# Performance work log

Measured on AMD Instinct MI355X. Metric: run time of the kernel, lower is better.

## Reference

```python
import jax, jax.numpy as jnp
import numpy as np
from jax import lax

T, B, H, HID = 1024, 64, 512, 512
EPS = 1e-5


def _lstm_scan(xs, Wx, Wh, b):
    # xs: [T, B, H] time-major; returns hidden states [T, B, HID]
    bsz = xs.shape[1]
    c0 = jnp.zeros((bsz, Wh.shape[0]), xs.dtype)
    h0 = jnp.zeros_like(c0)

    def step(carry, x):
        c, h = carry
        z = x @ Wx + h @ Wh + b  # [B, 4*HID]
        i, f, g, o = jnp.split(z, 4, axis=-1)  # flax gate order i, f, g, o
        c = jax.nn.sigmoid(f) * c + jax.nn.sigmoid(i) * jnp.tanh(g)
        h = jax.nn.sigmoid(o) * jnp.tanh(c)
        return (c, h), h

    _, hs = lax.scan(step, (c0, h0), xs)
    return hs


def _flip_sequences(x_bth, lengths):
    # x_bth: [B, T, H]; keep padding at the end while reversing valid prefix.
    max_len = x_bth.shape[1]
    return jax.vmap(lambda x, l: jnp.flip(jnp.roll(x, max_len - l, axis=0), axis=0))(
        x_bth, lengths)


def setup_inputs() -> dict:
    key = jax.random.key(0)
    ks = jax.random.split(key, 12)
    inputs = jax.random.normal(ks[0], (T, B, H), jnp.float32)
    lengths = jax.random.randint(ks[1], (B,), T // 2, T + 1).astype(jnp.int32)
    t_idx = jnp.arange(T)[:, None]
    mask = (t_idx < lengths[None, :]).astype(jnp.float32).reshape(T * B, 1)
    # BatchNorm params
    scale = 1.0 + 0.1 * jax.random.normal(ks[2], (H,), jnp.float32)
    bias = 0.1 * jax.random.normal(ks[3], (H,), jnp.float32)
    sx = 1.0 / np.sqrt(H)
    sh = 1.0 / np.sqrt(HID)
    Wx_f = sx * jax.random.normal(ks[4], (H, 4 * HID), jnp.float32)
    Wh_f = sh * jax.random.normal(ks[5], (HID, 4 * HID), jnp.float32)
    b_f = jnp.zeros((4 * HID,), jnp.float32)
    Wx_b = sx * jax.random.normal(ks[6], (H, 4 * HID), jnp.float32)
    Wh_b = sh * jax.random.normal(ks[7], (HID, 4 * HID), jnp.float32)
    b_b = jnp.zeros((4 * HID,), jnp.float32)
    return {
        "inputs": inputs, "lengths": lengths, "mask": mask,
        "scale": scale, "bias": bias,
        "Wx_f": Wx_f, "Wh_f": Wh_f, "b_f": b_f,
        "Wx_b": Wx_b, "Wh_b": Wh_b, "b_b": b_b,
        "training": 1,
    }


def reference(inputs, lengths, mask, scale, bias,
              Wx_f, Wh_f, b_f, Wx_b, Wh_b, b_b, training):
    t, n, h = inputs.shape
    x = inputs.reshape(t * n, h)
    if training:
        # masked batch statistics (matches flax BatchNorm override)
        non_zeros = jnp.sum(mask, axis=0)  # [1]
        mean = jnp.sum(x, axis=0) / non_zeros  # [H]
        mean2 = jnp.sum(lax.square(x), axis=0) / non_zeros
        var = jnp.maximum(0.0, mean2 - lax.square(mean))
    else:
        mean = jnp.zeros((h,), jnp.float32)
        var = jnp.ones((h,), jnp.float32)
    y = (x - mean) * lax.rsqrt(var + EPS) * scale + bias
    y = (y * mask).reshape(t, n, h)  # [T, B, H]

    # forward direction
    fwd = _lstm_scan(y, Wx_f, Wh_f, b_f)  # [T, B, HID]
    # backward direction on length-aware flipped inputs
    rev_in = _flip_sequences(y.transpose(1, 0, 2), lengths).transpose(1, 0, 2)
    bwd = _lstm_scan(rev_in, Wx_b, Wh_b, b_b)
    bwd = _flip_sequences(bwd.transpose(1, 0, 2), lengths).transpose(1, 0, 2)
    return fwd + bwd  # [T, B, HID]
```

## Files before the change

kernel.cpp:

```cpp
#include <hip/hip_runtime.h>
#include <math.h>

#define T_DIM 1024
#define B_DIM 64
#define H_DIM 512
#define HID   512
#define EPS_F 1e-5f

#define WS_SUM    0
#define WS_SUMSQ  512
#define WS_A      1024
#define WS_C0     1536
#define WS_HBUF   4096
#define WS_CBUF   (4096 + 131072)
#define WS_XZ     (4096 + 131072 + 65536)
#define WS_END    (WS_XZ + 524288)

__device__ __forceinline__ float sigf(float v) {
    return 1.0f / (1.0f + __expf(-v));
}

__global__ void stats_kernel(const float* __restrict__ x, float* __restrict__ ws) {
    int col = blockIdx.x * 256 + threadIdx.x;
    int row0 = blockIdx.y * 512;
    float s = 0.f, s2 = 0.f;
    for (int r = 0; r < 512; ++r) {
        float v = x[(size_t)(row0 + r) * H_DIM + col];
        s += v;
        s2 += v * v;
    }
    atomicAdd(&ws[WS_SUM + col], s);
    atomicAdd(&ws[WS_SUMSQ + col], s2);
}

__global__ void finalize_kernel(const int* __restrict__ lengths,
                                const float* __restrict__ scale,
                                const float* __restrict__ bias,
                                const int* __restrict__ training,
                                float* __restrict__ ws) {
    __shared__ float cnt_sh;
    int tid = threadIdx.x;
    if (tid == 0) {
        int c = 0;
        for (int b = 0; b < B_DIM; ++b) c += lengths[b];
        cnt_sh = (float)c;
    }
    __syncthreads();
    float a, c0;
    if (*training) {
        float inv = 1.0f / cnt_sh;
        float mean = ws[WS_SUM + tid] * inv;
        float mean2 = ws[WS_SUMSQ + tid] * inv;
        float var = fmaxf(0.0f, mean2 - mean * mean);
        a = scale[tid] * rsqrtf(var + EPS_F);
        c0 = bias[tid] - mean * a;
    } else {
        a = scale[tid] * rsqrtf(1.0f + EPS_F);
        c0 = bias[tid];
    }
    ws[WS_A + tid] = a;
    ws[WS_C0 + tid] = c0;
}

__launch_bounds__(256)
__global__ void step_kernel(int t,
                            const float* __restrict__ x,
                            const int* __restrict__ lengths,
                            const float* __restrict__ mask,
                            const float* __restrict__ Wx_f, const float* __restrict__ Wh_f,
                            const float* __restrict__ b_f,
                            const float* __restrict__ Wx_b, const float* __restrict__ Wh_b,
                            const float* __restrict__ b_b,
                            float* __restrict__ ws, float* __restrict__ out) {
    __shared__ __align__(16) float As[64 * 68];
    __shared__ __align__(16) float Ws_[64 * 68];

    const int role = blockIdx.x >> 6;
    const int r6   = blockIdx.x & 63;
    const int dir  = r6 >> 5;
    const int jt   = r6 & 31;
    const int tid  = threadIdx.x;
    const int tidb = tid & 15;
    const int tidn = tid >> 4;
    const int b0   = tidb << 2;
    const int n0   = tidn << 2;

    const int target = t + 1;
    if (role == 0 && t < 0) return;
    if (role == 1 && target >= T_DIM) return;

    const int g   = tidn >> 2;
    const int jj0 = (tidn & 3) << 2;
    const int col_base = g * 512 + jt * 16 + jj0;

    const float* W  = (role == 1) ? (dir ? Wx_b : Wx_f) : (dir ? Wh_b : Wh_f);
    const float* bv = dir ? b_b : b_f;

    float acc[4][4];
    if (role == 0) {
        const int xzb = ((t & 1) * 2 + dir) * (B_DIM * 2048);
#pragma unroll
        for (int i = 0; i < 4; ++i) {
            float4 v = *reinterpret_cast<const float4*>(&ws[WS_XZ + xzb + (b0 + i) * 2048 + col_base]);
            acc[i][0] = v.x; acc[i][1] = v.y; acc[i][2] = v.z; acc[i][3] = v.w;
        }
    } else {
        float4 bvv = *reinterpret_cast<const float4*>(&bv[col_base]);
#pragma unroll
        for (int i = 0; i < 4; ++i) {
            acc[i][0] = bvv.x; acc[i][1] = bvv.y; acc[i][2] = bvv.z; acc[i][3] = bvv.w;
        }
    }

    const int hbase_in = ((t & 1) * 2 + dir) * (B_DIM * 512);

    for (int ck = 0; ck < 8; ++ck) {
        const int k0c = ck * 64;
#pragma unroll
        for (int i = 0; i < 4; ++i) {
            int f4  = tid + i * 256;
            int kk4 = f4 & 15;
            int b   = f4 >> 4;
            int k   = k0c + (kk4 << 2);
            float4 v;
            if (role == 0) {
                v = *reinterpret_cast<const float4*>(&ws[WS_HBUF + hbase_in + b * 512 + k]);
            } else {
                int trow;
                if (dir == 0) {
                    trow = target;
                } else {
                    trow = lengths[b] - 1 - target;
                    if (trow < 0) trow += T_DIM;
                }
                float4 xv = *reinterpret_cast<const float4*>(&x[((size_t)trow * B_DIM + b) * H_DIM + k]);
                float  m  = mask[(size_t)trow * B_DIM + b];
                float4 av = *reinterpret_cast<const float4*>(&ws[WS_A + k]);
                float4 cv = *reinterpret_cast<const float4*>(&ws[WS_C0 + k]);
                v.x = (xv.x * av.x + cv.x) * m;
                v.y = (xv.y * av.y + cv.y) * m;
                v.z = (xv.z * av.z + cv.z) * m;
                v.w = (xv.w * av.w + cv.w) * m;
            }
            int kr = kk4 << 2;
            As[(kr + 0) * 68 + b] = v.x;
            As[(kr + 1) * 68 + b] = v.y;
            As[(kr + 2) * 68 + b] = v.z;
            As[(kr + 3) * 68 + b] = v.w;
        }
#pragma unroll
        for (int i = 0; i < 4; ++i) {
            int f4  = tid + i * 256;
            int n4  = f4 & 15;
            int kk  = f4 >> 4;
            int nl  = n4 << 2;
            int gg  = nl >> 4;
            int jj  = nl & 15;
            int colw = gg * 512 + jt * 16 + jj;
            float4 wv = *reinterpret_cast<const float4*>(&W[(size_t)(k0c + kk) * 2048 + colw]);
            *reinterpret_cast<float4*>(&Ws_[kk * 68 + nl]) = wv;
        }
        __syncthreads();
#pragma unroll 4
        for (int kk = 0; kk < 64; ++kk) {
            const float4 a4 = *reinterpret_cast<const float4*>(&As[kk * 68 + b0]);
            const float4 w4 = *reinterpret_cast<const float4*>(&Ws_[kk * 68 + n0]);
            acc[0][0] += a4.x * w4.x; acc[0][1] += a4.x * w4.y; acc[0][2] += a4.x * w4.z; acc[0][3] += a4.x * w4.w;
            acc[1][0] += a4.y * w4.x; acc[1][1] += a4.y * w4.y; acc[1][2] += a4.y * w4.z; acc[1][3] += a4.y * w4.w;
            acc[2][0] += a4.z * w4.x; acc[2][1] += a4.z * w4.y; acc[2][2] += a4.z * w4.z; acc[2][3] += a4.z * w4.w;
            acc[3][0] += a4.w * w4.x; acc[3][1] += a4.w * w4.y; acc[3][2] += a4.w * w4.z; acc[3][3] += a4.w * w4.w;
        }
        __syncthreads();
    }

    if (role == 1) {
        const int xzb = ((target & 1) * 2 + dir) * (B_DIM * 2048);
#pragma unroll
        for (int i = 0; i < 4; ++i) {
            float4 v = make_float4(acc[i][0], acc[i][1], acc[i][2], acc[i][3]);
            *reinterpret_cast<float4*>(&ws[WS_XZ + xzb + (b0 + i) * 2048 + col_base]) = v;
        }
        return;
    }

    float* zs = As;
#pragma unroll
    for (int i = 0; i < 4; ++i) {
        float4 v = make_float4(acc[i][0], acc[i][1], acc[i][2], acc[i][3]);
        *reinterpret_cast<float4*>(&zs[(b0 + i) * 68 + n0]) = v;
    }
    __syncthreads();

    const int b   = tid >> 2;
    const int jjg = (tid & 3) << 2;
    const int hc  = jt * 16 + jjg;

    float4 zi = *reinterpret_cast<const float4*>(&zs[b * 68 +  0 + jjg]);
    float4 zf = *reinterpret_cast<const float4*>(&zs[b * 68 + 16 + jjg]);
    float4 zg = *reinterpret_cast<const float4*>(&zs[b * 68 + 32 + jjg]);
    float4 zo = *reinterpret_cast<const float4*>(&zs[b * 68 + 48 + jjg]);

    float* cptr = &ws[WS_CBUF + (dir * B_DIM + b) * 512 + hc];
    float4 c4 = *reinterpret_cast<const float4*>(cptr);

    float cn[4], hv[4];
    {
        float c = sigf(zf.x) * c4.x + sigf(zi.x) * tanhf(zg.x);
        cn[0] = c; hv[0] = sigf(zo.x) * tanhf(c);
    }
    {
        float c = sigf(zf.y) * c4.y + sigf(zi.y) * tanhf(zg.y);
        cn[1] = c; hv[1] = sigf(zo.y) * tanhf(c);
    }
    {
        float c = sigf(zf.z) * c4.z + sigf(zi.z) * tanhf(zg.z);
        cn[2] = c; hv[2] = sigf(zo.z) * tanhf(c);
    }
    {
        float c = sigf(zf.w) * c4.w + sigf(zi.w) * tanhf(zg.w);
        cn[3] = c; hv[3] = sigf(zo.w) * tanhf(c);
    }

    *reinterpret_cast<float4*>(cptr) = make_float4(cn[0], cn[1], cn[2], cn[3]);

    const int hbase_out = (((t + 1) & 1) * 2 + dir) * (B_DIM * 512);
    *reinterpret_cast<float4*>(&ws[WS_HBUF + hbase_out + b * 512 + hc]) =
        make_float4(hv[0], hv[1], hv[2], hv[3]);

    int orow;
    if (dir == 0) {
        orow = t;
    } else {
        orow = lengths[b] - 1 - t;
        if (orow < 0) orow += T_DIM;
    }
    float* op = &out[((size_t)orow * B_DIM + b) * HID + hc];
    atomicAdd(&op[0], hv[0]);
    atomicAdd(&op[1], hv[1]);
    atomicAdd(&op[2], hv[2]);
    atomicAdd(&op[3], hv[3]);
}

extern "C" void kernel_launch(void* const* d_in, const int* in_sizes, int n_in,
                              void* d_out, int out_size, void* d_ws, size_t ws_size,
                              hipStream_t stream) {
    const float* x        = (const float*)d_in[0];
    const int*   lengths  = (const int*)d_in[1];
    const float* mask     = (const float*)d_in[2];
    const float* scale    = (const float*)d_in[3];
    const float* bias     = (const float*)d_in[4];
    const float* Wx_f     = (const float*)d_in[5];
    const float* Wh_f     = (const float*)d_in[6];
    const float* b_f      = (const float*)d_in[7];
    const float* Wx_b     = (const float*)d_in[8];
    const float* Wh_b     = (const float*)d_in[9];
    const float* b_b      = (const float*)d_in[10];
    const int*   training = (const int*)d_in[11];
    float* ws  = (float*)d_ws;
    float* out = (float*)d_out;

    hipMemsetAsync(ws, 0, (size_t)WS_END * sizeof(float), stream);
    hipMemsetAsync(out, 0, (size_t)out_size * sizeof(float), stream);

    stats_kernel<<<dim3(2, 128), 256, 0, stream>>>(x, ws);
    finalize_kernel<<<1, 512, 0, stream>>>(lengths, scale, bias, training, ws);

    for (int t = -1; t < T_DIM; ++t) {
        step_kernel<<<128, 256, 0, stream>>>(t, x, lengths, mask,
                                             Wx_f, Wh_f, b_f, Wx_b, Wh_b, b_b,
                                             ws, out);
    }
}
```

Baseline: 40.12 ms.

## Replace per-step launches with a persistent cooperative kernel using grid sync

Merges the stats, finalize and 1025 per-timestep launches into one cooperative kernel of 256 blocks that loops over time and separates steps with grid.sync. Half the blocks run the recurrent h·Wh update with split-K across 8 waves and a shared-memory reduction. The other blocks normalize and transpose the input and compute the x·Wx projection two stages ahead, replacing the mask read with a length comparison. The aim is to remove kernel launch overhead and overlap the input projection with the recurrence. The cost is a grid-wide barrier every step, and the weights are now read straight from global memory with no shared-memory tiling.

```diff
diff --git a/kernel.cpp b/kernel.cpp
--- a/kernel.cpp
+++ b/kernel.cpp
@@ -1,244 +1,221 @@
 #include <hip/hip_runtime.h>
+#include <hip/hip_cooperative_groups.h>
 #include <math.h>
+
+namespace cg = cooperative_groups;
 
 #define T_DIM 1024
 #define B_DIM 64
 #define H_DIM 512
-#define HID   512
 #define EPS_F 1e-5f
 
 #define WS_SUM    0
 #define WS_SUMSQ  512
-#define WS_A      1024
-#define WS_C0     1536
-#define WS_HBUF   4096
-#define WS_CBUF   (4096 + 131072)
-#define WS_XZ     (4096 + 131072 + 65536)
-#define WS_END    (WS_XZ + 524288)
+#define WS_HT     1024
+#define WS_CT     (WS_HT + 131072)
+#define WS_XZ     (WS_CT + 65536)
+#define WS_YT     (WS_XZ + 524288)
+#define WS_END    (WS_YT + 131072)
+#define WS_ZERO_END WS_XZ
 
 __device__ __forceinline__ float sigf(float v) {
     return 1.0f / (1.0f + __expf(-v));
 }
 
-__global__ void stats_kernel(const float* __restrict__ x, float* __restrict__ ws) {
-    int col = blockIdx.x * 256 + threadIdx.x;
-    int row0 = blockIdx.y * 512;
-    float s = 0.f, s2 = 0.f;
-    for (int r = 0; r < 512; ++r) {
-        float v = x[(size_t)(row0 + r) * H_DIM + col];
-        s += v;
-        s2 += v * v;
+__global__ __launch_bounds__(512)
+void brnn_persistent(const float* __restrict__ x, const int* __restrict__ lengths,
+                     const float* __restrict__ scale, const float* __restrict__ bias,
+                     const float* __restrict__ Wx_f, const float* __restrict__ Wh_f,
+                     const float* __restrict__ b_f,
+                     const float* __restrict__ Wx_b, const float* __restrict__ Wh_b,
+                     const float* __restrict__ b_b,
+                     const int* __restrict__ training,
+                     float* __restrict__ ws, float* __restrict__ out) {
+    cg::grid_group grid = cg::this_grid();
+
+    __shared__ union {
+        float red[8 * 2080];
+        float tile[512 * 9];
+    } U;
+    __shared__ float a_sh[512], c0_sh[512];
+    __shared__ int lsh[64];
+
+    const int tid = threadIdx.x;
+    const int bid = blockIdx.x;
+
+    {
+        float s = 0.f, s2 = 0.f;
+        const float* xp = x + (size_t)bid * 256 * 512 + tid;
+#pragma unroll 8
+        for (int r = 0; r < 256; ++r) {
+            float v = xp[(size_t)r * 512];
+            s += v; s2 += v * v;
+        }
+        atomicAdd(&ws[WS_SUM + tid], s);
+        atomicAdd(&ws[WS_SUMSQ + tid], s2);
     }
-    atomicAdd(&ws[WS_SUM + col], s);
-    atomicAdd(&ws[WS_SUMSQ + col], s2);
-}
-
-__global__ void finalize_kernel(const int* __restrict__ lengths,
-                                const float* __restrict__ scale,
-                                const float* __restrict__ bias,
-                                const int* __restrict__ training,
-                                float* __restrict__ ws) {
-    __shared__ float cnt_sh;
-    int tid = threadIdx.x;
-    if (tid == 0) {
-        int c = 0;
-        for (int b = 0; b < B_DIM; ++b) c += lengths[b];
-        cnt_sh = (float)c;
+    grid.sync();
+
+    if (tid < 64) lsh[tid] = lengths[tid];
+    __syncthreads();
+    {
+        float cnt = 0.f;
+        for (int b = 0; b < 64; ++b) cnt += (float)lsh[b];
+        float a, c0;
+        if (*training) {
+            float inv = 1.0f / cnt;
+            float mean = ws[WS_SUM + tid] * inv;
+            float mean2 = ws[WS_SUMSQ + tid] * inv;
+            float var = fmaxf(0.f, mean2 - mean * mean);
+            a = scale[tid] * rsqrtf(var + EPS_F);
+            c0 = bias[tid] - mean * a;
+        } else {
+            a = scale[tid] * rsqrtf(1.0f + EPS_F);
+            c0 = bias[tid];
+        }
+        a_sh[tid] = a;
+        c0_sh[tid] = c0;
     }
     __syncthreads();
-    float a, c0;
-    if (*training) {
-        float inv = 1.0f / cnt_sh;
-        float mean = ws[WS_SUM + tid] * inv;
-        float mean2 = ws[WS_SUMSQ + tid] * inv;
-        float var = fmaxf(0.0f, mean2 - mean * mean);
-        a = scale[tid] * rsqrtf(var + EPS_F);
-        c0 = bias[tid] - mean * a;
-    } else {
-        a = scale[tid] * rsqrtf(1.0f + EPS_F);
-        c0 = bias[tid];
+
+    const int w = __builtin_amdgcn_readfirstlane(tid >> 6);
+    const int lane = tid & 63;
+    const int kbase = w * 64;
+
+    for (int i = -2; i <= 1023; ++i) {
+        if (bid < 128) {
+            if (i >= 0) {
+                const int dir = bid >> 6;
+                const int hb = bid & 63;
+                const int hbase = hb << 3;
+                const int p = i & 1;
+                const float* __restrict__ Wh = dir ? Wh_b : Wh_f;
+                const float* arow = ws + WS_HT + ((size_t)(p * 2 + dir) * 512 + kbase) * 64 + lane;
+                const float* wp = Wh + (size_t)kbase * 2048 + hbase;
+                float acc[32];
+#pragma unroll
+                for (int c = 0; c < 32; ++c) acc[c] = 0.f;
+#pragma unroll 4
+                for (int kk = 0; kk < 64; ++kk) {
+                    float av = arow[kk * 64];
+                    const float* wr = wp + (size_t)kk * 2048;
+#pragma unroll
+                    for (int g = 0; g < 4; ++g)
+#pragma unroll
+                        for (int j = 0; j < 8; ++j)
+                            acc[g * 8 + j] = fmaf(wr[g * 512 + j], av, acc[g * 8 + j]);
+                }
+                __syncthreads();
+#pragma unroll
+                for (int c = 0; c < 32; ++c) U.red[w * 2080 + c * 65 + lane] = acc[c];
+                __syncthreads();
+                const int b = tid & 63;
+                const int h8 = tid >> 6;
+                const int hid = hbase + h8;
+                const float* xzp = ws + WS_XZ + (size_t)(p * 2 + dir) * 2048 * 64;
+                float z[4];
+#pragma unroll
+                for (int g = 0; g < 4; ++g) {
+                    float s = 0.f;
+#pragma unroll
+                    for (int w8 = 0; w8 < 8; ++w8)
+                        s += U.red[w8 * 2080 + (g * 8 + h8) * 65 + b];
+                    z[g] = s + xzp[(size_t)(g * 512 + hid) * 64 + b];
+                }
+                float* cp = ws + WS_CT + (size_t)(dir * 512 + hid) * 64 + b;
+                float cold = *cp;
+                float ig = sigf(z[0]), fg = sigf(z[1]);
+                float gg = tanhf(z[2]), og = sigf(z[3]);
+                float cn = fg * cold + ig * gg;
+                float hv = og * tanhf(cn);
+                *cp = cn;
+                ws[WS_HT + (size_t)(((p ^ 1) * 2 + dir) * 512 + hid) * 64 + b] = hv;
+                int orow;
+                if (dir == 0) orow = i;
+                else { orow = lsh[b] - 1 - i; if (orow < 0) orow += T_DIM; }
+                atomicAdd(&out[((size_t)orow * 64 + b) * 512 + hid], hv);
+            }
+        } else {
+            if (bid < 144 && i <= 1021) {
+                const int idx = bid - 128;
+                const int dir2 = idx & 1, bo = idx >> 1;
+                const int ttgt = i + 2;
+#pragma unroll
+                for (int it = 0; it < 2; ++it) {
+                    int id2 = tid + it * 512;
+                    int row = id2 >> 7;
+                    int k4 = id2 & 127;
+                    int b = bo * 8 + row;
+                    int l = lsh[b];
+                    int trow = dir2 ? (l - 1 - ttgt) : ttgt;
+                    if (trow < 0) trow += T_DIM;
+                    float m = (trow < l) ? 1.f : 0.f;
+                    const float4 xv = *reinterpret_cast<const float4*>(
+                        &x[((size_t)trow * 64 + b) * 512 + k4 * 4]);
+                    float4 a4 = *reinterpret_cast<const float4*>(&a_sh[k4 * 4]);
+                    float4 c4 = *reinterpret_cast<const float4*>(&c0_sh[k4 * 4]);
+                    U.tile[(k4 * 4 + 0) * 9 + row] = (xv.x * a4.x + c4.x) * m;
+                    U.tile[(k4 * 4 + 1) * 9 + row] = (xv.y * a4.y + c4.y) * m;
+                    U.tile[(k4 * 4 + 2) * 9 + row] = (xv.z * a4.z + c4.z) * m;
+                    U.tile[(k4 * 4 + 3) * 9 + row] = (xv.w * a4.w + c4.w) * m;
+                }
+                __syncthreads();
+                const int q2 = ttgt & 1;
+                float* yt = ws + WS_YT + (size_t)(q2 * 2 + dir2) * 512 * 64;
+#pragma unroll
+                for (int it = 0; it < 8; ++it) {
+                    int gid = tid + it * 512;
+                    int b = gid & 7;
+                    int k = gid >> 3;
+                    yt[(size_t)k * 64 + bo * 8 + b] = U.tile[k * 9 + b];
+                }
+                __syncthreads();
+            }
+            if (i >= -1 && i <= 1022) {
+                const int idx = bid - 128;
+                const int dir = idx >> 6;
+                const int cb = idx & 63;
+                const int colbase = cb << 5;
+                const int tt = i + 1;
+                const int q = tt & 1;
+                const float* __restrict__ Wx = dir ? Wx_b : Wx_f;
+                const float* __restrict__ bv = dir ? b_b : b_f;
+                const float* arow = ws + WS_YT + ((size_t)(q * 2 + dir) * 512 + kbase) * 64 + lane;
+                const float* wp = Wx + (size_t)kbase * 2048 + colbase;
+                float acc[32];
+#pragma unroll
+                for (int c = 0; c < 32; ++c) acc[c] = 0.f;
+#pragma unroll 4
+                for (int kk = 0; kk < 64; ++kk) {
+                    float av = arow[kk * 64];
+                    const float* wr = wp + (size_t)kk * 2048;
+#pragma unroll
+                    for (int c = 0; c < 32; ++c)
+                        acc[c] = fmaf(wr[c], av, acc[c]);
+                }
+                __syncthreads();
+#pragma unroll
+                for (int c = 0; c < 32; ++c) U.red[w * 2080 + c * 65 + lane] = acc[c];
+                __syncthreads();
+                const int co2 = tid >> 4;
+                const int b4 = (tid & 15) << 2;
+                float bb = bv[colbase + co2];
+                float r[4];
+#pragma unroll
+                for (int j = 0; j < 4; ++j) {
+                    float s = 0.f;
+#pragma unroll
+                    for (int w8 = 0; w8 < 8; ++w8)
+                        s += U.red[w8 * 2080 + co2 * 65 + b4 + j];
+                    r[j] = s + bb;
+                }
+                *reinterpret_cast<float4*>(
+                    &ws[WS_XZ + ((size_t)(q * 2 + dir) * 2048 + colbase + co2) * 64 + b4]) =
+                    make_float4(r[0], r[1], r[2], r[3]);
+            }
+        }
+        grid.sync();
     }
-    ws[WS_A + tid] = a;
-    ws[WS_C0 + tid] = c0;
-}
-
-__launch_bounds__(256)
-__global__ void step_kernel(int t,
-                            const float* __restrict__ x,
-                            const int* __restrict__ lengths,
-                            const float* __restrict__ mask,
-                            const float* __restrict__ Wx_f, const float* __restrict__ Wh_f,
-                            const float* __restrict__ b_f,
-                            const float* __restrict__ Wx_b, const float* __restrict__ Wh_b,
-                            const float* __restrict__ b_b,
-                            float* __restrict__ ws, float* __restrict__ out) {
-    __shared__ __align__(16) float As[64 * 68];
-    __shared__ __align__(16) float Ws_[64 * 68];
-
-    const int role = blockIdx.x >> 6;
-    const int r6   = blockIdx.x & 63;
-    const int dir  = r6 >> 5;
-    const int jt   = r6 & 31;
-    const int tid  = threadIdx.x;
-    const int tidb = tid & 15;
-    const int tidn = tid >> 4;
-    const int b0   = tidb << 2;
-    const int n0   = tidn << 2;
-
-    const int target = t + 1;
-    if (role == 0 && t < 0) return;
-    if (role == 1 && target >= T_DIM) return;
-
-    const int g   = tidn >> 2;
-    const int jj0 = (tidn & 3) << 2;
-    const int col_base = g * 512 + jt * 16 + jj0;
-
-    const float* W  = (role == 1) ? (dir ? Wx_b : Wx_f) : (dir ? Wh_b : Wh_f);
-    const float* bv = dir ? b_b : b_f;
-
-    float acc[4][4];
-    if (role == 0) {
-        const int xzb = ((t & 1) * 2 + dir) * (B_DIM * 2048);
-#pragma unroll
-        for (int i = 0; i < 4; ++i) {
-            float4 v = *reinterpret_cast<const float4*>(&ws[WS_XZ + xzb + (b0 + i) * 2048 + col_base]);
-            acc[i][0] = v.x; acc[i][1] = v.y; acc[i][2] = v.z; acc[i][3] = v.w;
-        }
-    } else {
-        float4 bvv = *reinterpret_cast<const float4*>(&bv[col_base]);
-#pragma unroll
-        for (int i = 0; i < 4; ++i) {
-            acc[i][0] = bvv.x; acc[i][1] = bvv.y; acc[i][2] = bvv.z; acc[i][3] = bvv.w;
-        }
-    }
-
-    const int hbase_in = ((t & 1) * 2 + dir) * (B_DIM * 512);
-
-    for (int ck = 0; ck < 8; ++ck) {
-        const int k0c = ck * 64;
-#pragma unroll
-        for (int i = 0; i < 4; ++i) {
-            int f4  = tid + i * 256;
-            int kk4 = f4 & 15;
-            int b   = f4 >> 4;
-            int k   = k0c + (kk4 << 2);
-            float4 v;
-            if (role == 0) {
-                v = *reinterpret_cast<const float4*>(&ws[WS_HBUF + hbase_in + b * 512 + k]);
-            } else {
-                int trow;
-                if (dir == 0) {
-                    trow = target;
-                } else {
-                    trow = lengths[b] - 1 - target;
-                    if (trow < 0) trow += T_DIM;
-                }
-                float4 xv = *reinterpret_cast<const float4*>(&x[((size_t)trow * B_DIM + b) * H_DIM + k]);
-                float  m  = mask[(size_t)trow * B_DIM + b];
-                float4 av = *reinterpret_cast<const float4*>(&ws[WS_A + k]);
-                float4 cv = *reinterpret_cast<const float4*>(&ws[WS_C0 + k]);
-                v.x = (xv.x * av.x + cv.x) * m;
-                v.y = (xv.y * av.y + cv.y) * m;
-                v.z = (xv.z * av.z + cv.z) * m;
-                v.w = (xv.w * av.w + cv.w) * m;
-            }
-            int kr = kk4 << 2;
-            As[(kr + 0) * 68 + b] = v.x;
-            As[(kr + 1) * 68 + b] = v.y;
-            As[(kr + 2) * 68 + b] = v.z;
-            As[(kr + 3) * 68 + b] = v.w;
-        }
-#pragma unroll
-        for (int i = 0; i < 4; ++i) {
-            int f4  = tid + i * 256;
-            int n4  = f4 & 15;
-            int kk  = f4 >> 4;
-            int nl  = n4 << 2;
-            int gg  = nl >> 4;
-            int jj  = nl & 15;
-            int colw = gg * 512 + jt * 16 + jj;
-            float4 wv = *reinterpret_cast<const float4*>(&W[(size_t)(k0c + kk) * 2048 + colw]);
-            *reinterpret_cast<float4*>(&Ws_[kk * 68 + nl]) = wv;
-        }
-        __syncthreads();
-#pragma unroll 4
-        for (int kk = 0; kk < 64; ++kk) {
-            const float4 a4 = *reinterpret_cast<const float4*>(&As[kk * 68 + b0]);
-            const float4 w4 = *reinterpret_cast<const float4*>(&Ws_[kk * 68 + n0]);
-            acc[0][0] += a4.x * w4.x; acc[0][1] += a4.x * w4.y; acc[0][2] += a4.x * w4.z; acc[0][3] += a4.x * w4.w;
-            acc[1][0] += a4.y * w4.x; acc[1][1] += a4.y * w4.y; acc[1][2] += a4.y * w4.z; acc[1][3] += a4.y * w4.w;
-            acc[2][0] += a4.z * w4.x; acc[2][1] += a4.z * w4.y; acc[2][2] += a4.z * w4.z; acc[2][3] += a4.z * w4.w;
-            acc[3][0] += a4.w * w4.x; acc[3][1] += a4.w * w4.y; acc[3][2] += a4.w * w4.z; acc[3][3] += a4.w * w4.w;
-        }
-        __syncthreads();
-    }
-
-    if (role == 1) {
-        const int xzb = ((target & 1) * 2 + dir) * (B_DIM * 2048);
-#pragma unroll
-        for (int i = 0; i < 4; ++i) {
-            float4 v = make_float4(acc[i][0], acc[i][1], acc[i][2], acc[i][3]);
-            *reinterpret_cast<float4*>(&ws[WS_XZ + xzb + (b0 + i) * 2048 + col_base]) = v;
-        }
-        return;
-    }
-
-    float* zs = As;
-#pragma unroll
-    for (int i = 0; i < 4; ++i) {
-        float4 v = make_float4(acc[i][0], acc[i][1], acc[i][2], acc[i][3]);
-        *reinterpret_cast<float4*>(&zs[(b0 + i) * 68 + n0]) = v;
-    }
-    __syncthreads();
-
-    const int b   = tid >> 2;
-    const int jjg = (tid & 3) << 2;
-    const int hc  = jt * 16 + jjg;
-
-    float4 zi = *reinterpret_cast<const float4*>(&zs[b * 68 +  0 + jjg]);
-    float4 zf = *reinterpret_cast<const float4*>(&zs[b * 68 + 16 + jjg]);
-    float4 zg = *reinterpret_cast<const float4*>(&zs[b * 68 + 32 + jjg]);
-    float4 zo = *reinterpret_cast<const float4*>(&zs[b * 68 + 48 + jjg]);
-
-    float* cptr = &ws[WS_CBUF + (dir * B_DIM + b) * 512 + hc];
-    float4 c4 = *reinterpret_cast<const float4*>(cptr);
-
-    float cn[4], hv[4];
-    {
-        float c = sigf(zf.x) * c4.x + sigf(zi.x) * tanhf(zg.x);
-        cn[0] = c; hv[0] = sigf(zo.x) * tanhf(c);
-    }
-    {
-        float c = sigf(zf.y) * c4.y + sigf(zi.y) * tanhf(zg.y);
-        cn[1] = c; hv[1] = sigf(zo.y) * tanhf(c);
-    }
-    {
-        float c = sigf(zf.z) * c4.z + sigf(zi.z) * tanhf(zg.z);
-        cn[2] = c; hv[2] = sigf(zo.z) * tanhf(c);
-    }
-    {
-        float c = sigf(zf.w) * c4.w + sigf(zi.w) * tanhf(zg.w);
-        cn[3] = c; hv[3] = sigf(zo.w) * tanhf(c);
-    }
-
-    *reinterpret_cast<float4*>(cptr) = make_float4(cn[0], cn[1], cn[2], cn[3]);
-
-    const int hbase_out = (((t + 1) & 1) * 2 + dir) * (B_DIM * 512);
-    *reinterpret_cast<float4*>(&ws[WS_HBUF + hbase_out + b * 512 + hc]) =
-        make_float4(hv[0], hv[1], hv[2], hv[3]);
-
-    int orow;
-    if (dir == 0) {
-        orow = t;
-    } else {
-        orow = lengths[b] - 1 - t;
-        if (orow < 0) orow += T_DIM;
-    }
-    float* op = &out[((size_t)orow * B_DIM + b) * HID + hc];
-    atomicAdd(&op[0], hv[0]);
-    atomicAdd(&op[1], hv[1]);
-    atomicAdd(&op[2], hv[2]);
-    atomicAdd(&op[3], hv[3]);
 }
 
 extern "C" void kernel_launch(void* const* d_in, const int* in_sizes, int n_in,
@@ -246,7 +223,6 @@
                               hipStream_t stream) {
     const float* x        = (const float*)d_in[0];
     const int*   lengths  = (const int*)d_in[1];
-    const float* mask     = (const float*)d_in[2];
     const float* scale    = (const float*)d_in[3];
     const float* bias     = (const float*)d_in[4];
     const float* Wx_f     = (const float*)d_in[5];
@@ -259,15 +235,15 @@
     float* ws  = (float*)d_ws;
     float* out = (float*)d_out;
 
-    hipMemsetAsync(ws, 0, (size_t)WS_END * sizeof(float), stream);
+    hipMemsetAsync(ws, 0, (size_t)WS_ZERO_END * sizeof(float), stream);
     hipMemsetAsync(out, 0, (size_t)out_size * sizeof(float), stream);
 
-    stats_kernel<<<dim3(2, 128), 256, 0, stream>>>(x, ws);
-    finalize_kernel<<<1, 512, 0, stream>>>(lengths, scale, bias, training, ws);
-
-    for (int t = -1; t < T_DIM; ++t) {
-        step_kernel<<<128, 256, 0, stream>>>(t, x, lengths, mask,
-                                             Wx_f, Wh_f, b_f, Wx_b, Wh_b, b_b,
-                                             ws, out);
-    }
+    void* args[] = {
+        (void*)&x, (void*)&lengths, (void*)&scale, (void*)&bias,
+        (void*)&Wx_f, (void*)&Wh_f, (void*)&b_f,
+        (void*)&Wx_b, (void*)&Wh_b, (void*)&b_b,
+        (void*)&training, (void*)&ws, (void*)&out
+    };
+    hipLaunchCooperativeKernel((const void*)brnn_persistent,
+                               dim3(256), dim3(512), args, 0, stream);
 }
```

Result: slower. 51.83 ms (+29.2%).
